# Kernel optimization log

Hardware: AMD Instinct MI355X
Metric: run time of the kernel (lower is better)

Reference implementation:

```python
import jax, jax.numpy as jnp
import numpy as np

N_NODES = 50000
NEG_SLOPE = 0.2


def gat_layer(x, src, dst, W, a_src, a_dst, b, concat):
    # x: [N, Fin]; W: [Fin, H*C]; a_src/a_dst: [H, C]; b: [H*C] or [C]
    H, C = a_src.shape
    h = (x @ W).reshape(-1, H, C)                      # [N, H, C]
    al_s = jnp.einsum('nhc,hc->nh', h, a_src)          # [N, H]
    al_d = jnp.einsum('nhc,hc->nh', h, a_dst)          # [N, H]
    e = jax.nn.leaky_relu(al_s[src] + al_d[dst], NEG_SLOPE)   # [E, H]
    # segment softmax over incoming edges of each destination node
    e_max = jax.ops.segment_max(e, dst, num_segments=N_NODES)  # [N, H]
    ex = jnp.exp(e - e_max[dst])
    denom = jax.ops.segment_sum(ex, dst, num_segments=N_NODES)
    alpha = ex / (denom[dst] + 1e-16)                  # [E, H]
    msg = h[src] * alpha[:, :, None]                   # [E, H, C]
    out = jax.ops.segment_sum(msg, dst, num_segments=N_NODES)  # [N, H, C]
    out = out.reshape(N_NODES, H * C) if concat else out.mean(axis=1)
    return out + b


def setup_inputs() -> dict:
    key = jax.random.key(0)
    ks = jax.random.split(key, 16)
    x = jax.random.normal(ks[0], (N_NODES, 12), dtype=jnp.float32)
    edge_index = jax.random.randint(ks[1], (2, 400000), 0, N_NODES, dtype=jnp.int32)
    H, C = 8, 64
    s = 0.1
    W1 = jax.random.normal(ks[2], (12, H * C), jnp.float32) * s
    as1 = jax.random.normal(ks[3], (H, C), jnp.float32) * s
    ad1 = jax.random.normal(ks[4], (H, C), jnp.float32) * s
    b1 = jnp.zeros((H * C,), jnp.float32)
    W2 = jax.random.normal(ks[5], (H * C, H * C), jnp.float32) * s
    as2 = jax.random.normal(ks[6], (H, C), jnp.float32) * s
    ad2 = jax.random.normal(ks[7], (H, C), jnp.float32) * s
    b2 = jnp.zeros((H * C,), jnp.float32)
    W3 = jax.random.normal(ks[8], (H * C, H * 5), jnp.float32) * s
    as3 = jax.random.normal(ks[9], (H, 5), jnp.float32) * s
    ad3 = jax.random.normal(ks[10], (H, 5), jnp.float32) * s
    b3 = jnp.zeros((5,), jnp.float32)
    return {"x": x, "edge_index": edge_index,
            "W1": W1, "as1": as1, "ad1": ad1, "b1": b1,
            "W2": W2, "as2": as2, "ad2": ad2, "b2": b2,
            "W3": W3, "as3": as3, "ad3": ad3, "b3": b3}


def reference(x, edge_index, W1, as1, ad1, b1, W2, as2, ad2, b2, W3, as3, ad3, b3):
    # add self-loops (PyG GATConv default add_self_loops=True)
    loop = jnp.arange(N_NODES, dtype=edge_index.dtype)
    src = jnp.concatenate([edge_index[0], loop])
    dst = jnp.concatenate([edge_index[1], loop])
    h = gat_layer(x, src, dst, W1, as1, ad1, b1, concat=True)
    h = jax.nn.relu(h)
    h = gat_layer(h, src, dst, W2, as2, ad2, b2, concat=True)
    h = jax.nn.relu(h)
    h = gat_layer(h, src, dst, W3, as3, ad3, b3, concat=False)
    return jax.nn.log_softmax(h, axis=1)
```

## Files before the change

kernel.cpp:

```cpp
#include <hip/hip_runtime.h>
#include <hip/hip_bf16.h>

#define NN    50000
#define MP    50048
#define E0C   400000
#define ETOT  450000
#define HH    8
#define FF    512
#define F3    40
#define C3    5
#define MAXE  128
#define NBLK  ((NN + 1023) / 1024)
#define MT2   (MP / 128)
#define GT2   (MT2 * 4)

typedef __attribute__((ext_vector_type(8))) short bf16x8;
typedef __attribute__((ext_vector_type(8))) short s16x8;
typedef __attribute__((ext_vector_type(4))) float f32x4;

__device__ inline unsigned short f2bf(float f) {
    union { float f; unsigned int u; } v; v.f = f;
    unsigned int r = v.u + 0x7FFF + ((v.u >> 16) & 1);
    return (unsigned short)(r >> 16);
}
__device__ inline float bf2f(unsigned short u) {
    union { unsigned int i; float f; } v; v.i = ((unsigned int)u) << 16;
    return v.f;
}

__global__ void count_kernel(const int* __restrict__ ei, int* __restrict__ cnt) {
    int e = blockIdx.x * blockDim.x + threadIdx.x;
    if (e >= ETOT) return;
    int dst = (e < E0C) ? ei[E0C + e] : (e - E0C);
    atomicAdd(&cnt[dst], 1);
}

__global__ __launch_bounds__(1024) void scan_blocks(int* __restrict__ cnt,
                                                    int* __restrict__ offs,
                                                    int* __restrict__ bsum) {
    __shared__ int s[1024];
    int tid = threadIdx.x;
    int i = blockIdx.x * 1024 + tid;
    int v = (i < NN) ? cnt[i] : 0;
    if (i < NN) cnt[i] = 0;
    s[tid] = v;
    __syncthreads();
    for (int d = 1; d < 1024; d <<= 1) {
        int add = (tid >= d) ? s[tid - d] : 0;
        __syncthreads();
        s[tid] += add;
        __syncthreads();
    }
    if (i < NN) offs[i + 1] = s[tid];
    if (tid == 1023) bsum[blockIdx.x] = s[1023];
}

__global__ __launch_bounds__(1024) void scan_add(int* __restrict__ offs,
                                                 const int* __restrict__ bsum) {
    __shared__ int pref;
    int tid = threadIdx.x;
    if (tid < 64) {
        int v = (tid < blockIdx.x) ? bsum[tid] : 0;
#pragma unroll
        for (int d = 32; d; d >>= 1) v += __shfl_xor(v, d);
        if (tid == 0) pref = v;
    }
    __syncthreads();
    int i = blockIdx.x * 1024 + tid;
    if (i < NN) offs[i + 1] += pref;
    if (i == 0) offs[0] = 0;
}

__global__ void scatter_kernel(const int* __restrict__ ei, const int* __restrict__ offs,
                               int* __restrict__ cur, int* __restrict__ srcs) {
    int e = blockIdx.x * blockDim.x + threadIdx.x;
    if (e >= ETOT) return;
    int src, dst;
    if (e < E0C) { src = ei[e]; dst = ei[E0C + e]; }
    else         { src = dst = e - E0C; }
    int pos = offs[dst] + atomicAdd(&cur[dst], 1);
    srcs[pos] = src;
}

__global__ void prep_all(const float* __restrict__ W2, const float* __restrict__ W3,
                         unsigned short* __restrict__ W2T, unsigned short* __restrict__ W3T,
                         unsigned short* __restrict__ A2) {
    int i = blockIdx.x * blockDim.x + threadIdx.x;
    if (i < FF * FF) {
        int n = i >> 9, k = i & 511;
        W2T[i] = f2bf(W2[k * FF + n]);
        return;
    }
    int j = i - FF * FF;
    if (j < 48 * 512) {
        int n = j >> 9, k = j & 511;
        W3T[j] = (n < F3) ? f2bf(W3[k * F3 + n]) : 0;
        return;
    }
    int l = j - 48 * 512;
    if (l < (MP - NN) * FF) A2[(size_t)NN * FF + l] = 0;
}

__global__ __launch_bounds__(256) void gemm1_fused(
    const float* __restrict__ x, const float* __restrict__ W1,
    const float* __restrict__ as1, const float* __restrict__ ad1,
    unsigned short* __restrict__ hb, float* __restrict__ al_s,
    float* __restrict__ al_d) {
    __shared__ float xs[64 * 12];
    int t = threadIdx.x;
    int n0 = blockIdx.x * 64;
    int nvalid = NN - n0; if (nvalid > 64) nvalid = 64;

    for (int j = t; j < nvalid * 12; j += 256) xs[j] = x[(size_t)n0 * 12 + j];
    __syncthreads();

    int f = t * 2;
    float w0[12], w1[12];
#pragma unroll
    for (int k = 0; k < 12; ++k) {
        float2 wv = *(const float2*)&W1[k * FF + f];
        w0[k] = wv.x; w1[k] = wv.y;
    }
    float2 asv = *(const float2*)&as1[f];
    float2 adv = *(const float2*)&ad1[f];
    int head = t >> 5;

    for (int ni = 0; ni < nvalid; ++ni) {
        const float* xp = &xs[ni * 12];
        float4 xa = *(const float4*)xp;
        float4 xb = *(const float4*)(xp + 4);
        float4 xc = *(const float4*)(xp + 8);
        float xv[12] = {xa.x, xa.y, xa.z, xa.w, xb.x, xb.y, xb.z, xb.w,
                        xc.x, xc.y, xc.z, xc.w};
        float h0 = 0.f, h1 = 0.f;
#pragma unroll
        for (int k = 0; k < 12; ++k) { h0 += xv[k] * w0[k]; h1 += xv[k] * w1[k]; }
        unsigned int u = ((unsigned int)f2bf(h1) << 16) | f2bf(h0);
        *(unsigned int*)&hb[(size_t)(n0 + ni) * FF + f] = u;
        float ps = h0 * asv.x + h1 * asv.y;
        float pd = h0 * adv.x + h1 * adv.y;
#pragma unroll
        for (int d = 1; d < 32; d <<= 1) {
            ps += __shfl_xor(ps, d);
            pd += __shfl_xor(pd, d);
        }
        if ((t & 31) == 0) {
            al_s[(size_t)(n0 + ni) * HH + head] = ps;
            al_d[(size_t)(n0 + ni) * HH + head] = pd;
        }
    }
}

__global__ __launch_bounds__(256) void attn_gather(
    const unsigned short* __restrict__ Hb,
    const float* __restrict__ alS, const float* __restrict__ alD,
    const int* __restrict__ offs, const int* __restrict__ srcs,
    const float* __restrict__ bias,
    float* __restrict__ out_f32, unsigned short* __restrict__ out_b16, int relu) {
    __shared__ float alpha_sh[4][MAXE][HH];
    __shared__ int   srcs_sh[4][MAXE];
    int w = threadIdx.x >> 6, lane = threadIdx.x & 63;
    int n = blockIdx.x * 4 + w;
    if (n >= NN) return;
    int h = lane >> 3, es = lane & 7;
    int beg = offs[n], end = offs[n + 1], deg = end - beg;

    float ald = alD[n * HH + h];
    float m = -1e30f, den = 0.f, idn;

    if (deg <= MAXE) {
        for (int e = es; e < deg; e += 8) {
            int s = srcs[beg + e];
            if (h == 0) srcs_sh[w][e] = s;
            float sc = alS[s * HH + h] + ald;
            sc = sc > 0.f ? sc : 0.2f * sc;
            alpha_sh[w][e][h] = sc;
            m = fmaxf(m, sc);
        }
        m = fmaxf(m, __shfl_xor(m, 1));
        m = fmaxf(m, __shfl_xor(m, 2));
        m = fmaxf(m, __shfl_xor(m, 4));
        for (int e = es; e < deg; e += 8) {
            float ex = __expf(alpha_sh[w][e][h] - m);
            den += ex;
            alpha_sh[w][e][h] = ex;
        }
        den += __shfl_xor(den, 1);
        den += __shfl_xor(den, 2);
        den += __shfl_xor(den, 4);
        idn = 1.f / (den + 1e-16f);
    } else {
        for (int e = es; e < deg; e += 8) {
            int s = srcs[beg + e];
            float sc = alS[s * HH + h] + ald;
            sc = sc > 0.f ? sc : 0.2f * sc;
            m = fmaxf(m, sc);
        }
        m = fmaxf(m, __shfl_xor(m, 1));
        m = fmaxf(m, __shfl_xor(m, 2));
        m = fmaxf(m, __shfl_xor(m, 4));
        for (int e = es; e < deg; e += 8) {
            int s = srcs[beg + e];
            float sc = alS[s * HH + h] + ald;
            sc = sc > 0.f ? sc : 0.2f * sc;
            den += __expf(sc - m);
        }
        den += __shfl_xor(den, 1);
        den += __shfl_xor(den, 2);
        den += __shfl_xor(den, 4);
        idn = 1.f / (den + 1e-16f);
    }

    int f0 = lane * 8;
    float acc[8] = {};
    if (deg <= MAXE) {
        int e = 0;
        for (; e + 4 <= deg; e += 4) {
            int s0 = srcs_sh[w][e + 0], s1 = srcs_sh[w][e + 1];
            int s2 = srcs_sh[w][e + 2], s3 = srcs_sh[w][e + 3];
            bf16x8 v0 = *(const bf16x8*)&Hb[(size_t)s0 * FF + f0];
            bf16x8 v1 = *(const bf16x8*)&Hb[(size_t)s1 * FF + f0];
            bf16x8 v2 = *(const bf16x8*)&Hb[(size_t)s2 * FF + f0];
            bf16x8 v3 = *(const bf16x8*)&Hb[(size_t)s3 * FF + f0];
            float a0 = alpha_sh[w][e + 0][h], a1 = alpha_sh[w][e + 1][h];
            float a2 = alpha_sh[w][e + 2][h], a3 = alpha_sh[w][e + 3][h];
#pragma unroll
            for (int k = 0; k < 8; ++k) {
                acc[k] += a0 * bf2f((unsigned short)v0[k]);
                acc[k] += a1 * bf2f((unsigned short)v1[k]);
                acc[k] += a2 * bf2f((unsigned short)v2[k]);
                acc[k] += a3 * bf2f((unsigned short)v3[k]);
            }
        }
        for (; e < deg; ++e) {
            int s = srcs_sh[w][e];
            float a = alpha_sh[w][e][h];
            bf16x8 v = *(const bf16x8*)&Hb[(size_t)s * FF + f0];
#pragma unroll
            for (int k = 0; k < 8; ++k)
                acc[k] += a * bf2f((unsigned short)v[k]);
        }
#pragma unroll
        for (int k = 0; k < 8; ++k) acc[k] *= idn;
    } else {
        for (int e = 0; e < deg; ++e) {
            int s = srcs[beg + e];
            float sc = alS[s * HH + h] + ald;
            sc = sc > 0.f ? sc : 0.2f * sc;
            float a = __expf(sc - m) * idn;
            bf16x8 v = *(const bf16x8*)&Hb[(size_t)s * FF + f0];
#pragma unroll
            for (int k = 0; k < 8; ++k)
                acc[k] += a * bf2f((unsigned short)v[k]);
        }
    }
    float4 b0 = *(const float4*)&bias[f0];
    float4 b1 = *(const float4*)&bias[f0 + 4];
    float bv[8] = {b0.x, b0.y, b0.z, b0.w, b1.x, b1.y, b1.z, b1.w};
    float vv[8];
#pragma unroll
    for (int k = 0; k < 8; ++k) {
        float t = acc[k] + bv[k];
        vv[k] = relu ? fmaxf(t, 0.f) : t;
    }
    if (out_f32) {
        float4 o0 = {vv[0], vv[1], vv[2], vv[3]};
        float4 o1 = {vv[4], vv[5], vv[6], vv[7]};
        *(float4*)&out_f32[(size_t)n * FF + f0] = o0;
        *(float4*)&out_f32[(size_t)n * FF + f0 + 4] = o1;
    }
    if (out_b16) {
        s16x8 ov;
#pragma unroll
        for (int k = 0; k < 8; ++k) ov[k] = (short)f2bf(vv[k]);
        *(s16x8*)&out_b16[(size_t)n * FF + f0] = ov;
    }
}

__global__ __launch_bounds__(256) void gemm_mfma(
    const unsigned short* __restrict__ A,
    const unsigned short* __restrict__ BT,
    const float* __restrict__ a_s, const float* __restrict__ a_d,
    unsigned short* __restrict__ Cb,
    float* __restrict__ alS, float* __restrict__ alD,
    int N, int K) {
    __shared__ unsigned short As[2][128 * 64];
    __shared__ unsigned short Bs[2][128 * 64];
    int t = threadIdx.x;
    int wave = t >> 6, lane = t & 63;
    int wr = wave >> 1, wc = wave & 1;

    int bid = blockIdx.x;
    int mt, nt;
    if (bid < (MT2 / 8) * 32) {
        int g = bid >> 5, r = bid & 31;
        mt = g * 8 + (r & 7);
        nt = r >> 3;
    } else {
        int t2 = bid - (MT2 / 8) * 32;
        mt = (MT2 / 8) * 8 + (t2 >> 2);
        nt = t2 & 3;
    }
    int m0 = mt * 128, n0 = nt * 128;

    f32x4 acc[4][4] = {};
    int kg = lane >> 4;
    int lr = lane & 15;

    auto STAGE = [&](int buf, int k0) {
#pragma unroll
        for (int q = 0; q < 4; ++q) {
            int c   = q * 256 + t;
            int row = c >> 3, kc = c & 7;
            int kcs = kc ^ (row & 7);
            const unsigned short* ga = A + (size_t)(m0 + row) * K + k0 + kcs * 8;
            const unsigned short* gb = BT + (size_t)(n0 + row) * K + k0 + kcs * 8;
            unsigned short* la = &As[buf][(size_t)(q * 256 + wave * 64) * 8];
            unsigned short* lb = &Bs[buf][(size_t)(q * 256 + wave * 64) * 8];
            __builtin_amdgcn_global_load_lds(
                (const __attribute__((address_space(1))) void*)ga,
                (__attribute__((address_space(3))) void*)la, 16, 0, 0);
            __builtin_amdgcn_global_load_lds(
                (const __attribute__((address_space(1))) void*)gb,
                (__attribute__((address_space(3))) void*)lb, 16, 0, 0);
        }
    };

    const int NT = K / 64;
    STAGE(0, 0);
    __syncthreads();
    int cur = 0;
    for (int kt = 0; kt < NT; ++kt) {
        if (kt + 1 < NT) STAGE(cur ^ 1, (kt + 1) * 64);
        const unsigned short* Ac = As[cur];
        const unsigned short* Bc = Bs[cur];
#pragma unroll
        for (int ks = 0; ks < 2; ++ks) {
            bf16x8 af[4], bf[4];
#pragma unroll
            for (int i = 0; i < 4; ++i) {
                int rowa = wr * 64 + i * 16 + lr;
                af[i] = *(const bf16x8*)&Ac[rowa * 64 + (((ks << 2) | kg) ^ (rowa & 7)) * 8];
                int rowb = wc * 64 + i * 16 + lr;
                bf[i] = *(const bf16x8*)&Bc[rowb * 64 + (((ks << 2) | kg) ^ (rowb & 7)) * 8];
            }
#pragma unroll
            for (int i = 0; i < 4; ++i)
#pragma unroll
                for (int j = 0; j < 4; ++j)
                    acc[i][j] = __builtin_amdgcn_mfma_f32_16x16x32_bf16(
                        af[i], bf[j], acc[i][j], 0, 0, 0);
        }
        __syncthreads();
        cur ^= 1;
    }

    int head = (n0 >> 6) + wc;
    float asv[4], adv[4];
#pragma unroll
    for (int j = 0; j < 4; ++j) {
        int cc = n0 + wc * 64 + j * 16 + lr;
        asv[j] = a_s[cc];
        adv[j] = a_d[cc];
    }
#pragma unroll
    for (int i = 0; i < 4; ++i) {
#pragma unroll
        for (int reg = 0; reg < 4; ++reg) {
            float ps = 0.f, pd = 0.f;
#pragma unroll
            for (int j = 0; j < 4; ++j) {
                ps += acc[i][j][reg] * asv[j];
                pd += acc[i][j][reg] * adv[j];
            }
#pragma unroll
            for (int d = 1; d < 16; d <<= 1) {
                ps += __shfl_xor(ps, d);
                pd += __shfl_xor(pd, d);
            }
            if (lr == 0) {
                int r = m0 + wr * 64 + i * 16 + kg * 4 + reg;
                alS[(size_t)r * HH + head] = ps;
                alD[(size_t)r * HH + head] = pd;
            }
        }
    }

#pragma unroll
    for (int i = 0; i < 4; ++i) {
        int rb = m0 + wr * 64 + i * 16 + kg * 4;
#pragma unroll
        for (int j = 0; j < 4; ++j) {
            int cc = n0 + wc * 64 + j * 16 + lr;
#pragma unroll
            for (int reg = 0; reg < 4; ++reg)
                Cb[(size_t)(rb + reg) * N + cc] = f2bf(acc[i][j][reg]);
        }
    }
}

__global__ __launch_bounds__(256) void gemm3_mfma(
    const unsigned short* __restrict__ A,
    const unsigned short* __restrict__ BT,
    float* __restrict__ C) {
    __shared__ unsigned short As[128 * 64];
    __shared__ unsigned short Bs[48 * 64];
    int t = threadIdx.x;
    int wave = t >> 6, lane = t & 63;
    int m0 = blockIdx.x * 128;
    int kg = lane >> 4, lr = lane & 15;

    f32x4 acc[2][3] = {};

    for (int k0 = 0; k0 < 512; k0 += 64) {
#pragma unroll
        for (int q = 0; q < 4; ++q) {
            int c   = q * 256 + t;
            int row = c >> 3, kc = c & 7;
            int kcs = kc ^ (row & 7);
            const unsigned short* ga = A + (size_t)(m0 + row) * 512 + k0 + kcs * 8;
            unsigned short* la = &As[(size_t)(q * 256 + wave * 64) * 8];
            __builtin_amdgcn_global_load_lds(
                (const __attribute__((address_space(1))) void*)ga,
                (__attribute__((address_space(3))) void*)la, 16, 0, 0);
        }
        {
            int c   = t;
            int row = c >> 3, kc = c & 7;
            int kcs = kc ^ (row & 7);
            const unsigned short* gb = BT + (size_t)row * 512 + k0 + kcs * 8;
            unsigned short* lb = &Bs[(size_t)(wave * 64) * 8];
            __builtin_amdgcn_global_load_lds(
                (const __attribute__((address_space(1))) void*)gb,
                (__attribute__((address_space(3))) void*)lb, 16, 0, 0);
        }
        if (t < 128) {
            int c   = 256 + t;
            int row = c >> 3, kc = c & 7;
            int kcs = kc ^ (row & 7);
            const unsigned short* gb = BT + (size_t)row * 512 + k0 + kcs * 8;
            unsigned short* lb = &Bs[(size_t)(256 + wave * 64) * 8];
            __builtin_amdgcn_global_load_lds(
                (const __attribute__((address_space(1))) void*)gb,
                (__attribute__((address_space(3))) void*)lb, 16, 0, 0);
        }
        __syncthreads();
#pragma unroll
        for (int ks = 0; ks < 2; ++ks) {
            bf16x8 af[2], bf[3];
#pragma unroll
            for (int i = 0; i < 2; ++i) {
                int rowa = wave * 32 + i * 16 + lr;
                af[i] = *(const bf16x8*)&As[rowa * 64 + (((ks << 2) | kg) ^ (rowa & 7)) * 8];
            }
#pragma unroll
            for (int j = 0; j < 3; ++j) {
                int rowb = j * 16 + lr;
                bf[j] = *(const bf16x8*)&Bs[rowb * 64 + (((ks << 2) | kg) ^ (rowb & 7)) * 8];
            }
#pragma unroll
            for (int i = 0; i < 2; ++i)
#pragma unroll
                for (int j = 0; j < 3; ++j)
                    acc[i][j] = __builtin_amdgcn_mfma_f32_16x16x32_bf16(
                        af[i], bf[j], acc[i][j], 0, 0, 0);
        }
        __syncthreads();
    }

#pragma unroll
    for (int i = 0; i < 2; ++i) {
        int rb = m0 + wave * 32 + i * 16 + kg * 4;
#pragma unroll
        for (int j = 0; j < 3; ++j) {
            int cc = j * 16 + lr;
            if (cc >= F3) continue;
#pragma unroll
            for (int reg = 0; reg < 4; ++reg) {
                int r = rb + reg;
                if (r < NN) C[(size_t)r * F3 + cc] = acc[i][j][reg];
            }
        }
    }
}

__global__ void al40_kernel(const float* __restrict__ h3, const float* __restrict__ as3,
                            const float* __restrict__ ad3, float* __restrict__ al_s,
                            float* __restrict__ al_d) {
    int n = blockIdx.x * blockDim.x + threadIdx.x;
    if (n >= NN) return;
#pragma unroll
    for (int hh = 0; hh < HH; ++hh) {
        float s = 0.f, d = 0.f;
#pragma unroll
        for (int c = 0; c < C3; ++c) {
            float v = h3[(size_t)n * F3 + hh * C3 + c];
            s += v * as3[hh * C3 + c];
            d += v * ad3[hh * C3 + c];
        }
        al_s[n * HH + hh] = s;
        al_d[n * HH + hh] = d;
    }
}

__global__ __launch_bounds__(256) void attn3_kernel(
    const float* __restrict__ h3, const float* __restrict__ al_s,
    const float* __restrict__ al_d, const int* __restrict__ offs,
    const int* __restrict__ srcs, const float* __restrict__ b3,
    float* __restrict__ out) {
    __shared__ float alpha_sh[4][MAXE][HH];
    __shared__ int   srcs_sh[4][MAXE];
    __shared__ float idn_sh[4][HH], m_sh[4][HH], ald_sh2[4][HH];
    __shared__ float accs[4][F3];
    __shared__ float vv[4][C3];
    int w = threadIdx.x >> 6, lane = threadIdx.x & 63;
    int n = blockIdx.x * 4 + w;
    int h = lane >> 3, es = lane & 7;
    int beg = offs[n], end = offs[n + 1], deg = end - beg;

    float ald = al_d[n * HH + h];
    float m = -1e30f, den = 0.f, idn;
    if (deg <= MAXE) {
        for (int e = es; e < deg; e += 8) {
            int s = srcs[beg + e];
            if (h == 0) srcs_sh[w][e] = s;
            float sc = al_s[s * HH + h] + ald;
            sc = sc > 0.f ? sc : 0.2f * sc;
            alpha_sh[w][e][h] = sc;
            m = fmaxf(m, sc);
        }
        m = fmaxf(m, __shfl_xor(m, 1));
        m = fmaxf(m, __shfl_xor(m, 2));
        m = fmaxf(m, __shfl_xor(m, 4));
        for (int e = es; e < deg; e += 8) {
            float ex = __expf(alpha_sh[w][e][h] - m);
            den += ex;
            alpha_sh[w][e][h] = ex;
        }
        den += __shfl_xor(den, 1);
        den += __shfl_xor(den, 2);
        den += __shfl_xor(den, 4);
        idn = 1.f / (den + 1e-16f);
        if (es == 0) idn_sh[w][h] = idn;
    } else {
        for (int e = es; e < deg; e += 8) {
            int s = srcs[beg + e];
            float sc = al_s[s * HH + h] + ald;
            sc = sc > 0.f ? sc : 0.2f * sc;
            m = fmaxf(m, sc);
        }
        m = fmaxf(m, __shfl_xor(m, 1));
        m = fmaxf(m, __shfl_xor(m, 2));
        m = fmaxf(m, __shfl_xor(m, 4));
        for (int e = es; e < deg; e += 8) {
            int s = srcs[beg + e];
            float sc = al_s[s * HH + h] + ald;
            sc = sc > 0.f ? sc : 0.2f * sc;
            den += __expf(sc - m);
        }
        den += __shfl_xor(den, 1);
        den += __shfl_xor(den, 2);
        den += __shfl_xor(den, 4);
        idn = 1.f / (den + 1e-16f);
        if (es == 0) { idn_sh[w][h] = idn; m_sh[w][h] = m; ald_sh2[w][h] = ald; }
    }
    __syncthreads();

    if (lane < F3) {
        int hh = lane / C3;
        float acc = 0.f;
        if (deg <= MAXE) {
            int e = 0;
            for (; e + 4 <= deg; e += 4) {
                int s0 = srcs_sh[w][e + 0], s1 = srcs_sh[w][e + 1];
                int s2 = srcs_sh[w][e + 2], s3 = srcs_sh[w][e + 3];
                float v0 = h3[(size_t)s0 * F3 + lane];
                float v1 = h3[(size_t)s1 * F3 + lane];
                float v2 = h3[(size_t)s2 * F3 + lane];
                float v3 = h3[(size_t)s3 * F3 + lane];
                acc += alpha_sh[w][e + 0][hh] * v0 + alpha_sh[w][e + 1][hh] * v1
                     + alpha_sh[w][e + 2][hh] * v2 + alpha_sh[w][e + 3][hh] * v3;
            }
            for (; e < deg; ++e) {
                int s = srcs_sh[w][e];
                acc += alpha_sh[w][e][hh] * h3[(size_t)s * F3 + lane];
            }
        } else {
            float mm = m_sh[w][hh], aald = ald_sh2[w][hh];
            for (int e = 0; e < deg; ++e) {
                int s = srcs[beg + e];
                float sc = al_s[s * HH + hh] + aald;
                sc = sc > 0.f ? sc : 0.2f * sc;
                acc += __expf(sc - mm) * h3[(size_t)s * F3 + lane];
            }
        }
        accs[w][lane] = acc * idn_sh[w][hh];
    }
    __syncthreads();
    if (lane < C3) {
        float s = 0.f;
#pragma unroll
        for (int hh = 0; hh < HH; ++hh) s += accs[w][hh * C3 + lane];
        vv[w][lane] = s * 0.125f + b3[lane];
    }
    __syncthreads();
    if (lane < C3) {
        float mx = vv[w][0];
#pragma unroll
        for (int c = 1; c < C3; ++c) mx = fmaxf(mx, vv[w][c]);
        float se = 0.f;
#pragma unroll
        for (int c = 0; c < C3; ++c) se += __expf(vv[w][c] - mx);
        out[(size_t)n * C3 + lane] = vv[w][lane] - mx - logf(se);
    }
}

extern "C" void kernel_launch(void* const* d_in, const int* in_sizes, int n_in,
                              void* d_out, int out_size, void* d_ws, size_t ws_size,
                              hipStream_t stream) {
    const float* x   = (const float*)d_in[0];
    const int*   ei  = (const int*)d_in[1];
    const float* W1  = (const float*)d_in[2];
    const float* as1 = (const float*)d_in[3];
    const float* ad1 = (const float*)d_in[4];
    const float* b1  = (const float*)d_in[5];
    const float* W2  = (const float*)d_in[6];
    const float* as2 = (const float*)d_in[7];
    const float* ad2 = (const float*)d_in[8];
    const float* b2  = (const float*)d_in[9];
    const float* W3  = (const float*)d_in[10];
    const float* as3 = (const float*)d_in[11];
    const float* ad3 = (const float*)d_in[12];
    const float* b3  = (const float*)d_in[13];
    float* out = (float*)d_out;

    auto au = [](size_t v) { return (v + 255) & ~(size_t)255; };
    char* p = (char*)d_ws;
    size_t szHb = au((size_t)MP * FF * 2);
    char* r1 = p;
    unsigned short* Hb1 = (unsigned short*)r1;
    unsigned short* Hb2 = (unsigned short*)r1;
    p += szHb;
    char* r2 = p;
    unsigned short* A2   = (unsigned short*)r2;
    unsigned short* Bb16 = (unsigned short*)r2;
    unsigned short* W2T  = (unsigned short*)(r2 + szHb);
    p = r2 + szHb + au((size_t)FF * FF * 2);
    unsigned short* W3T = (unsigned short*)p;  p += au((size_t)48 * 512 * 2);
    float* alS  = (float*)p;  p += au((size_t)MP * HH * 4);
    float* alD  = (float*)p;  p += au((size_t)MP * HH * 4);
    float* h3   = (float*)p;  p += au((size_t)NN * F3 * 4);
    int* offs   = (int*)p;    p += au((size_t)(NN + 1) * 4);
    int* cnt    = (int*)p;    p += au((size_t)NN * 4);
    int* srcs   = (int*)p;    p += au((size_t)ETOT * 4);
    int* bsum   = (int*)p;    p += au(64 * 4);

    hipMemsetAsync(cnt, 0, (size_t)NN * 4, stream);
    count_kernel<<<(ETOT + 255) / 256, 256, 0, stream>>>(ei, cnt);
    scan_blocks<<<NBLK, 1024, 0, stream>>>(cnt, offs, bsum);
    scan_add<<<NBLK, 1024, 0, stream>>>(offs, bsum);
    scatter_kernel<<<(ETOT + 255) / 256, 256, 0, stream>>>(ei, offs, cnt, srcs);
    {
        int prep_elems = FF * FF + 48 * 512 + (MP - NN) * FF;
        prep_all<<<(prep_elems + 255) / 256, 256, 0, stream>>>(W2, W3, W2T, W3T, A2);
    }

    gemm1_fused<<<(NN + 63) / 64, 256, 0, stream>>>(x, W1, as1, ad1, Hb1, alS, alD);
    attn_gather<<<(NN + 3) / 4, 256, 0, stream>>>(Hb1, alS, alD, offs, srcs, b1,
                                                  nullptr, A2, 1);

    gemm_mfma<<<GT2, 256, 0, stream>>>(
        A2, W2T, as2, ad2, Hb2, alS, alD, FF, FF);
    attn_gather<<<(NN + 3) / 4, 256, 0, stream>>>(Hb2, alS, alD, offs, srcs, b2,
                                                  nullptr, Bb16, 1);

    gemm3_mfma<<<MP / 128, 256, 0, stream>>>(Bb16, W3T, h3);
    al40_kernel<<<(NN + 255) / 256, 256, 0, stream>>>(h3, as3, ad3, alS, alD);
    attn3_kernel<<<NN / 4, 256, 0, stream>>>(h3, alS, alD, offs, srcs, b3, out);
}
```

Measured before the change: 344.8 us.

## Run layer-1 projection on MFMA GEMM and fuse layer-3 attention logits into GEMM3

The scalar FP32 layer-1 projection kernel is replaced by the existing bf16 MFMA GEMM path. For this, x is padded to K=64 and converted to bf16, and W1 is transposed, all in the prep kernel. Separately, GEMM3 now stages its output tile in shared memory and computes the per-head source and destination attention logits itself, which removes the separate al40 kernel and its reread of h3. The cost is extra prep work and memory for the padded bf16 x, plus wasted MFMA work on zero-padded K, and x now loses precision to bf16.

```diff
diff --git a/kernel.cpp b/kernel.cpp
--- a/kernel.cpp
+++ b/kernel.cpp
@@ -83,7 +83,9 @@
 }
 
 __global__ void prep_all(const float* __restrict__ W2, const float* __restrict__ W3,
+                         const float* __restrict__ W1, const float* __restrict__ x,
                          unsigned short* __restrict__ W2T, unsigned short* __restrict__ W3T,
+                         unsigned short* __restrict__ W1T, unsigned short* __restrict__ xb,
                          unsigned short* __restrict__ A2) {
     int i = blockIdx.x * blockDim.x + threadIdx.x;
     if (i < FF * FF) {
@@ -91,63 +93,27 @@
         W2T[i] = f2bf(W2[k * FF + n]);
         return;
     }
-    int j = i - FF * FF;
-    if (j < 48 * 512) {
-        int n = j >> 9, k = j & 511;
-        W3T[j] = (n < F3) ? f2bf(W3[k * F3 + n]) : 0;
+    i -= FF * FF;
+    if (i < 48 * 512) {
+        int n = i >> 9, k = i & 511;
+        W3T[i] = (n < F3) ? f2bf(W3[k * F3 + n]) : 0;
         return;
     }
-    int l = j - 48 * 512;
-    if (l < (MP - NN) * FF) A2[(size_t)NN * FF + l] = 0;
-}
-
-__global__ __launch_bounds__(256) void gemm1_fused(
-    const float* __restrict__ x, const float* __restrict__ W1,
-    const float* __restrict__ as1, const float* __restrict__ ad1,
-    unsigned short* __restrict__ hb, float* __restrict__ al_s,
-    float* __restrict__ al_d) {
-    __shared__ float xs[64 * 12];
-    int t = threadIdx.x;
-    int n0 = blockIdx.x * 64;
-    int nvalid = NN - n0; if (nvalid > 64) nvalid = 64;
-
-    for (int j = t; j < nvalid * 12; j += 256) xs[j] = x[(size_t)n0 * 12 + j];
-    __syncthreads();
-
-    int f = t * 2;
-    float w0[12], w1[12];
-#pragma unroll
-    for (int k = 0; k < 12; ++k) {
-        float2 wv = *(const float2*)&W1[k * FF + f];
-        w0[k] = wv.x; w1[k] = wv.y;
-    }
-    float2 asv = *(const float2*)&as1[f];
-    float2 adv = *(const float2*)&ad1[f];
-    int head = t >> 5;
-
-    for (int ni = 0; ni < nvalid; ++ni) {
-        const float* xp = &xs[ni * 12];
-        float4 xa = *(const float4*)xp;
-        float4 xb = *(const float4*)(xp + 4);
-        float4 xc = *(const float4*)(xp + 8);
-        float xv[12] = {xa.x, xa.y, xa.z, xa.w, xb.x, xb.y, xb.z, xb.w,
-                        xc.x, xc.y, xc.z, xc.w};
-        float h0 = 0.f, h1 = 0.f;
-#pragma unroll
-        for (int k = 0; k < 12; ++k) { h0 += xv[k] * w0[k]; h1 += xv[k] * w1[k]; }
-        unsigned int u = ((unsigned int)f2bf(h1) << 16) | f2bf(h0);
-        *(unsigned int*)&hb[(size_t)(n0 + ni) * FF + f] = u;
-        float ps = h0 * asv.x + h1 * asv.y;
-        float pd = h0 * adv.x + h1 * adv.y;
-#pragma unroll
-        for (int d = 1; d < 32; d <<= 1) {
-            ps += __shfl_xor(ps, d);
-            pd += __shfl_xor(pd, d);
-        }
-        if ((t & 31) == 0) {
-            al_s[(size_t)(n0 + ni) * HH + head] = ps;
-            al_d[(size_t)(n0 + ni) * HH + head] = pd;
-        }
+    i -= 48 * 512;
+    if (i < (MP - NN) * FF) {
+        A2[(size_t)NN * FF + i] = 0;
+        return;
+    }
+    i -= (MP - NN) * FF;
+    if (i < 512 * 64) {
+        int n = i >> 6, k = i & 63;
+        W1T[i] = (k < 12) ? f2bf(W1[k * FF + n]) : 0;
+        return;
+    }
+    i -= 512 * 64;
+    if (i < MP * 64) {
+        int r = i >> 6, k = i & 63;
+        xb[i] = (r < NN && k < 12) ? f2bf(x[r * 12 + k]) : 0;
     }
 }
 
@@ -402,9 +368,12 @@
 __global__ __launch_bounds__(256) void gemm3_mfma(
     const unsigned short* __restrict__ A,
     const unsigned short* __restrict__ BT,
-    float* __restrict__ C) {
+    const float* __restrict__ as3, const float* __restrict__ ad3,
+    float* __restrict__ C,
+    float* __restrict__ alS, float* __restrict__ alD) {
     __shared__ unsigned short As[128 * 64];
     __shared__ unsigned short Bs[48 * 64];
+    __shared__ float cls[128][F3];
     int t = threadIdx.x;
     int wave = t >> 6, lane = t & 63;
     int m0 = blockIdx.x * 128;
@@ -470,36 +439,35 @@
 
 #pragma unroll
     for (int i = 0; i < 2; ++i) {
-        int rb = m0 + wave * 32 + i * 16 + kg * 4;
+        int rloc = wave * 32 + i * 16 + kg * 4;
 #pragma unroll
         for (int j = 0; j < 3; ++j) {
             int cc = j * 16 + lr;
             if (cc >= F3) continue;
 #pragma unroll
             for (int reg = 0; reg < 4; ++reg) {
-                int r = rb + reg;
+                int rl = rloc + reg;
+                cls[rl][cc] = acc[i][j][reg];
+                int r = m0 + rl;
                 if (r < NN) C[(size_t)r * F3 + cc] = acc[i][j][reg];
             }
         }
     }
-}
-
-__global__ void al40_kernel(const float* __restrict__ h3, const float* __restrict__ as3,
-                            const float* __restrict__ ad3, float* __restrict__ al_s,
-                            float* __restrict__ al_d) {
-    int n = blockIdx.x * blockDim.x + threadIdx.x;
-    if (n >= NN) return;
-#pragma unroll
-    for (int hh = 0; hh < HH; ++hh) {
+    __syncthreads();
+
+    for (int p2 = t; p2 < 128 * HH; p2 += 256) {
+        int rl = p2 >> 3, hh = p2 & 7;
+        int r = m0 + rl;
+        if (r >= NN) continue;
         float s = 0.f, d = 0.f;
 #pragma unroll
         for (int c = 0; c < C3; ++c) {
-            float v = h3[(size_t)n * F3 + hh * C3 + c];
+            float v = cls[rl][hh * C3 + c];
             s += v * as3[hh * C3 + c];
             d += v * ad3[hh * C3 + c];
         }
-        al_s[n * HH + hh] = s;
-        al_d[n * HH + hh] = d;
+        alS[(size_t)r * HH + hh] = s;
+        alD[(size_t)r * HH + hh] = d;
     }
 }
 
@@ -647,6 +615,8 @@
     unsigned short* W2T  = (unsigned short*)(r2 + szHb);
     p = r2 + szHb + au((size_t)FF * FF * 2);
     unsigned short* W3T = (unsigned short*)p;  p += au((size_t)48 * 512 * 2);
+    unsigned short* W1T = (unsigned short*)p;  p += au((size_t)512 * 64 * 2);
+    unsigned short* xb  = (unsigned short*)p;  p += au((size_t)MP * 64 * 2);
     float* alS  = (float*)p;  p += au((size_t)MP * HH * 4);
     float* alD  = (float*)p;  p += au((size_t)MP * HH * 4);
     float* h3   = (float*)p;  p += au((size_t)NN * F3 * 4);
@@ -661,11 +631,14 @@
     scan_add<<<NBLK, 1024, 0, stream>>>(offs, bsum);
     scatter_kernel<<<(ETOT + 255) / 256, 256, 0, stream>>>(ei, offs, cnt, srcs);
     {
-        int prep_elems = FF * FF + 48 * 512 + (MP - NN) * FF;
-        prep_all<<<(prep_elems + 255) / 256, 256, 0, stream>>>(W2, W3, W2T, W3T, A2);
-    }
-
-    gemm1_fused<<<(NN + 63) / 64, 256, 0, stream>>>(x, W1, as1, ad1, Hb1, alS, alD);
+        long long prep_elems = (long long)FF * FF + 48 * 512 + (long long)(MP - NN) * FF
+                             + 512 * 64 + (long long)MP * 64;
+        prep_all<<<(int)((prep_elems + 255) / 256), 256, 0, stream>>>(
+            W2, W3, W1, x, W2T, W3T, W1T, xb, A2);
+    }
+
+    gemm_mfma<<<GT2, 256, 0, stream>>>(
+        xb, W1T, as1, ad1, Hb1, alS, alD, FF, 64);
     attn_gather<<<(NN + 3) / 4, 256, 0, stream>>>(Hb1, alS, alD, offs, srcs, b1,
                                                   nullptr, A2, 1);
 
@@ -674,7 +647,6 @@
     attn_gather<<<(NN + 3) / 4, 256, 0, stream>>>(Hb2, alS, alD, offs, srcs, b2,
                                                   nullptr, Bb16, 1);
 
-    gemm3_mfma<<<MP / 128, 256, 0, stream>>>(Bb16, W3T, h3);
-    al40_kernel<<<(NN + 255) / 256, 256, 0, stream>>>(h3, as3, ad3, alS, alD);
+    gemm3_mfma<<<MP / 128, 256, 0, stream>>>(Bb16, W3T, as3, ad3, h3, alS, alD);
     attn3_kernel<<<NN / 4, 256, 0, stream>>>(h3, alS, alD, offs, srcs, b3, out);
 }
```

Result: faster. 335.4 us (-2.7%).
